# Optimization experiments

Hardware: AMD Instinct MI355X
Metric: run time of the kernel (lower is better)

## Reference

```python
import jax, jax.numpy as jnp
import numpy as np

B, S, D_IN, D_Q, D_V, H = 2, 2048, 1024, 1024, 1024, 16
HD_Q, HD_V = D_Q // H, D_V // H
SCALE = float(D_Q) ** 0.5  # source scales by sqrt(d_q), NOT sqrt(head_dim)


def setup_inputs() -> dict:
    key = jax.random.key(0)
    k1, k2, k3, k4, k5 = jax.random.split(key, 5)
    return {
        "x": jax.random.normal(k1, (B, S, D_IN), dtype=jnp.float32),
        "w_q": jax.random.normal(k2, (D_IN, D_Q), dtype=jnp.float32),
        "w_k": jax.random.normal(k3, (D_IN, D_Q), dtype=jnp.float32),
        "w_v": jax.random.normal(k4, (D_IN, D_V), dtype=jnp.float32),
        "W_o": jax.random.normal(k5, (D_IN, D_V), dtype=jnp.float32),
    }


def reference(x, w_q, w_k, w_v, W_o):
    b, s, _ = x.shape
    # projections: [b, s, d]
    q = x @ w_q
    k = x @ w_k
    v = x @ w_v
    # split heads -> [b, h, s, hd]
    Q = q.reshape(b, s, H, HD_Q).transpose(0, 2, 1, 3)
    K = k.reshape(b, s, H, HD_Q).transpose(0, 2, 1, 3)
    V = v.reshape(b, s, H, HD_V).transpose(0, 2, 1, 3)
    # full [b, h, s, s] score matrix (naive attention, as in source)
    scores = jnp.einsum("bhqd,bhkd->bhqk", Q, K)
    # FAITHFUL QUIRK: source applies softmax over dim=0 (batch axis)
    attn = jax.nn.softmax(scores / SCALE, axis=0)
    vals = jnp.einsum("bhqk,bhkd->bhqd", attn, V)
    vals = vals.transpose(0, 2, 1, 3).reshape(b, s, D_V)
    return vals @ W_o
```

## Files before the change

### kernel.cpp

```cpp
#include <hip/hip_runtime.h>


typedef _Float16 f16;
typedef __attribute__((ext_vector_type(8))) _Float16 f16x8;
typedef __attribute__((ext_vector_type(4))) _Float16 f16x4;
typedef __attribute__((ext_vector_type(4))) float f32x4;

#define MFMA16(a,b,c) __builtin_amdgcn_mfma_f32_16x16x32_f16(a,b,c,0,0,0)
#define GLD16(gp, lp) __builtin_amdgcn_global_load_lds(                         \
    (const __attribute__((address_space(1))) void*)(gp),                        \
    (__attribute__((address_space(3))) void*)(lp), 16, 0, 0)

__global__ __launch_bounds__(256) void prep(const float* __restrict__ x,
                                            const float* __restrict__ w0, const float* __restrict__ w1,
                                            const float* __restrict__ w2, const float* __restrict__ w3,
                                            f16* __restrict__ xh,
                                            f16* __restrict__ o0, f16* __restrict__ o1,
                                            f16* __restrict__ o2, f16* __restrict__ o3) {
    const int bb = blockIdx.x;
    const int tid = threadIdx.x;
    if (bb >= 1024) {
        int i = (bb - 1024) * 256 + tid;
        float4 v = ((const float4*)x)[i];
        f16x4 h;
        h[0] = (f16)v.x; h[1] = (f16)v.y; h[2] = (f16)v.z; h[3] = (f16)v.w;
        *(f16x4*)(xh + (long)i * 4) = h;
        return;
    }
    const float* w; f16* o;
    switch (bb & 3) {
        case 0: w = w0; o = o0; break;
        case 1: w = w1; o = o1; break;
        case 2: w = w2; o = o2; break;
        default: w = w3; o = o3; break;
    }
    __shared__ alignas(16) f16 t[64][72];
    const int d0 = ((bb >> 2) & 15) * 64, j0 = (bb >> 6) * 64;
    #pragma unroll
    for (int it = 0; it < 4; ++it) {
        int idx = it * 256 + tid;
        int row = idx >> 4, c4 = idx & 15;
        float4 v = *(const float4*)(w + (long)(d0 + row) * 1024 + j0 + c4 * 4);
        f16x4 h;
        h[0] = (f16)v.x; h[1] = (f16)v.y; h[2] = (f16)v.z; h[3] = (f16)v.w;
        *(f16x4*)&t[row][c4 * 4] = h;
    }
    __syncthreads();
    #pragma unroll
    for (int it = 0; it < 4; ++it) {
        int idx = it * 256 + tid;
        int jr = idx >> 4, d4 = idx & 15;
        f16x4 h;
        #pragma unroll
        for (int m = 0; m < 4; ++m) h[m] = t[d4 * 4 + m][jr];
        *(f16x4*)(o + (long)(j0 + jr) * 1024 + d0 + d4 * 4) = h;
    }
}

__global__ __launch_bounds__(256, 1) void gemm_qkv(const f16* __restrict__ A,
                                                   const f16* __restrict__ Wt,
                                                   f16* __restrict__ Qg,
                                                   f16* __restrict__ Kg,
                                                   f16* __restrict__ Vtg) {
    __shared__ alignas(16) f16 smem[16384];
    f16* As = smem;
    f16* Bs = smem + 8192;
    const int tid = threadIdx.x;
    const int wave = tid >> 6, lane = tid & 63;
    const int l15 = lane & 15, lq = lane >> 4;
    const int sw = l15 & 7;
    const int m0 = blockIdx.x * 128, n0 = blockIdx.y * 128;
    const int wr = (wave >> 1) * 64, wc = (wave & 1) * 64;
    const int r8 = lane >> 3;
    const int swc8 = ((lane & 7) ^ r8) * 8;

    f32x4 acc[4][4] = {};

    for (int kt = 0; kt < 16; ++kt) {
        __syncthreads();
        #pragma unroll
        for (int i = 0; i < 4; ++i) {
            GLD16(A  + (long)(m0 + wave * 32 + i * 8 + r8) * 1024 + kt * 64 + swc8, As + (wave * 32 + i * 8) * 64);
            GLD16(Wt + (long)(n0 + wave * 32 + i * 8 + r8) * 1024 + kt * 64 + swc8, Bs + (wave * 32 + i * 8) * 64);
        }
        __syncthreads();
        #pragma unroll
        for (int s2 = 0; s2 < 2; ++s2) {
            const int rc = ((s2 * 4 + lq) ^ sw) << 3;
            f16x8 af[4], bf[4];
            #pragma unroll
            for (int i = 0; i < 4; ++i) af[i] = *(const f16x8*)&As[(wr + i * 16 + l15) * 64 + rc];
            #pragma unroll
            for (int j = 0; j < 4; ++j) bf[j] = *(const f16x8*)&Bs[(wc + j * 16 + l15) * 64 + rc];
            #pragma unroll
            for (int i = 0; i < 4; ++i)
                #pragma unroll
                for (int j = 0; j < 4; ++j)
                    acc[i][j] = MFMA16(af[i], bf[j], acc[i][j]);
        }
    }

    const int sel = n0 >> 10;
    const int nb = n0 - (sel << 10);

    if (sel < 2) {
        f16* dst = sel == 0 ? Qg : Kg;
        const float qs = sel == 0 ? 0.045084219f : 1.0f;
        __syncthreads();
        #pragma unroll
        for (int i = 0; i < 4; ++i)
            #pragma unroll
            for (int j = 0; j < 4; ++j) {
                int row0 = wr + i * 16 + lq * 4;
                int colb = wc + j * 16 + l15;
                int chunk = colb >> 3, sub = colb & 7;
                #pragma unroll
                for (int r = 0; r < 4; ++r) {
                    int row = row0 + r;
                    smem[row * 128 + ((chunk ^ (row & 7)) << 3) + sub] = (f16)(acc[i][j][r] * qs);
                }
            }
        __syncthreads();
        #pragma unroll
        for (int e = 0; e < 8; ++e) {
            int id = e * 256 + tid;
            int row = id >> 4, c = id & 15;
            f16x8 v = *(const f16x8*)&smem[row * 128 + ((c ^ (row & 7)) << 3)];
            int gr = m0 + row, b = gr >> 11, s = gr & 2047;
            int gc = nb + c * 8, hh = gc >> 6, hd = gc & 63;
            *(f16x8*)(dst + (long)((b * 16 + hh) * 2048 + s) * 64 + hd) = v;
        }
    } else {
        #pragma unroll
        for (int i = 0; i < 4; ++i)
            #pragma unroll
            for (int j = 0; j < 4; ++j) {
                int gr0 = m0 + wr + i * 16 + lq * 4;
                int gc  = nb + wc + j * 16 + l15;
                int b = gr0 >> 11, s = gr0 & 2047;
                int hh = gc >> 6, hd = gc & 63;
                f16x4 v;
                #pragma unroll
                for (int r = 0; r < 4; ++r) v[r] = (f16)acc[i][j][r];
                *(f16x4*)(Vtg + (long)((b * 16 + hh) * 64 + hd) * 2048 + s) = v;
            }
    }
}

__global__ __launch_bounds__(256, 1) void gemm_out(const f16* __restrict__ A0,
                                                   const f16* __restrict__ A1,
                                                   const f16* __restrict__ Bt,
                                                   float* __restrict__ outp) {
    __shared__ alignas(16) f16 As[64][72];
    __shared__ alignas(16) f16 Bs[128][64];
    const int tid = threadIdx.x;
    const int wave = tid >> 6, lane = tid & 63;
    const int l15 = lane & 15, lq = lane >> 4;
    const int sw = l15 & 7;
    const int m0 = blockIdx.x * 64, n0 = blockIdx.y * 128;
    const int wr = (wave >> 1) * 32, wc = (wave & 1) * 64;
    const int r8 = lane >> 3;
    const int swc8 = ((lane & 7) ^ r8) * 8;

    f32x4 acc[2][4] = {};

    for (int kt = 0; kt < 16; ++kt) {
        __syncthreads();
        #pragma unroll
        for (int it = 0; it < 2; ++it) {
            int idx = it * 256 + tid;
            int row = idx >> 3, c = idx & 7;
            f16x8 a = *(const f16x8*)(A0 + (long)(m0 + row) * 1024 + kt * 64 + c * 8)
                    + *(const f16x8*)(A1 + (long)(m0 + row) * 1024 + kt * 64 + c * 8);
            *(f16x8*)&As[row][c * 8] = a;
        }
        #pragma unroll
        for (int i = 0; i < 4; ++i)
            GLD16(Bt + (long)(n0 + wave * 32 + i * 8 + r8) * 1024 + kt * 64 + swc8, &Bs[wave * 32 + i * 8][0]);
        __syncthreads();
        #pragma unroll
        for (int s2 = 0; s2 < 2; ++s2) {
            const int rc = ((s2 * 4 + lq) ^ sw) << 3;
            f16x8 af[2], bf[4];
            #pragma unroll
            for (int i = 0; i < 2; ++i) af[i] = *(const f16x8*)&As[wr + i * 16 + l15][s2 * 32 + lq * 8];
            #pragma unroll
            for (int j = 0; j < 4; ++j) bf[j] = *(const f16x8*)&Bs[wc + j * 16 + l15][rc];
            #pragma unroll
            for (int i = 0; i < 2; ++i)
                #pragma unroll
                for (int j = 0; j < 4; ++j)
                    acc[i][j] = MFMA16(af[i], bf[j], acc[i][j]);
        }
    }

    #pragma unroll
    for (int i = 0; i < 2; ++i)
        #pragma unroll
        for (int j = 0; j < 4; ++j) {
            int gr0 = m0 + wr + i * 16 + lq * 4;
            int gc  = n0 + wc + j * 16 + l15;
            #pragma unroll
            for (int r = 0; r < 4; ++r)
                outp[(long)(gr0 + r) * 1024 + gc] = acc[i][j][r];
        }
}

__global__ __launch_bounds__(256, 2) void attention_kernel(const f16* __restrict__ Qg,
                                                           const f16* __restrict__ Kg,
                                                           const f16* __restrict__ Vtg,
                                                           f16* __restrict__ vals0,
                                                           f16* __restrict__ vals1) {
    __shared__ alignas(16) f16 Ks [2][2][64][64];
    __shared__ alignas(16) f16 Vts[2][2][64][64];
    __shared__ alignas(16) f16 Ps [4][32][64];
    const int tid = threadIdx.x;
    const int wave = tid >> 6, lane = tid & 63;
    const int l15 = lane & 15, lq = lane >> 4;
    const int sw = l15 & 7;

    const int bid = blockIdx.x;
    const int xcd = bid & 7, sl = bid >> 3;
    const int h  = xcd * 2 + (sl & 1);
    const int qt = (sl >> 1) & 15, ks = sl >> 5;
    const int q0 = qt * 128, kt0 = ks * 16;
    f16* vals = ks ? vals1 : vals0;
    const int qr = q0 + wave * 32;

    f16x8 qfr[2][2][2];
    #pragma unroll
    for (int b2 = 0; b2 < 2; ++b2)
        #pragma unroll
        for (int qq = 0; qq < 2; ++qq)
            #pragma unroll
            for (int s2 = 0; s2 < 2; ++s2)
                qfr[b2][qq][s2] = *(const f16x8*)(Qg + (long)((b2 * 16 + h) * 2048 + qr + qq * 16 + l15) * 64
                                                  + s2 * 32 + lq * 8);

    f32x4 acc[2][2][4] = {};

    const int tb = wave & 1;
    const int r8 = lane >> 3;
    const int swc8 = ((lane & 7) ^ r8) * 8;
    const f16* kbase = Kg  + (long)((tb * 16 + h) * 2048 + kt0 * 64) * 64 + r8 * 64 + swc8;
    const f16* vbase = Vtg + (long)((tb * 16 + h) * 64 + r8) * 2048 + kt0 * 64 + swc8;

    auto stage = [&](int kt, int buf) {
        if (wave < 2) {
            const f16* g = kbase + kt * 4096;
            f16* l = &Ks[buf][tb][0][0];
            #pragma unroll
            for (int i = 0; i < 8; ++i) GLD16(g + i * 512, l + i * 512);
        } else {
            const f16* g = vbase + kt * 64;
            f16* l = &Vts[buf][tb][0][0];
            #pragma unroll
            for (int i = 0; i < 8; ++i) GLD16(g + (long)i * 8 * 2048, l + i * 512);
        }
    };

    stage(0, 0);
    for (int kt = 0; kt < 16; ++kt) {
        const int cur = kt & 1;
        __syncthreads();
        if (kt < 15) stage(kt + 1, cur ^ 1);

        f16x4 pp0[2][4], pp1[2][4];
        #pragma unroll
        for (int kf = 0; kf < 4; ++kf) {
            f32x4 S0[2] = {}, S1[2] = {};
            #pragma unroll
            for (int s2 = 0; s2 < 2; ++s2) {
                const int rc = ((s2 * 4 + lq) ^ sw) << 3;
                f16x8 a0 = *(const f16x8*)&Ks[cur][0][kf * 16 + l15][rc];
                f16x8 a1 = *(const f16x8*)&Ks[cur][1][kf * 16 + l15][rc];
                #pragma unroll
                for (int qq = 0; qq < 2; ++qq) {
                    S0[qq] = MFMA16(a0, qfr[0][qq][s2], S0[qq]);
                    S1[qq] = MFMA16(a1, qfr[1][qq][s2], S1[qq]);
                }
            }
            #pragma unroll
            for (int qq = 0; qq < 2; ++qq)
                #pragma unroll
                for (int r = 0; r < 4; ++r) {
                    float e = __builtin_amdgcn_exp2f(S1[qq][r] - S0[qq][r]);
                    float p = __builtin_amdgcn_rcpf(1.0f + e);
                    pp0[qq][kf][r] = (f16)p;
                    pp1[qq][kf][r] = (f16)(1.0f - p);
                }
        }

        const int pwsub = (lq & 1) << 2;
        #pragma unroll
        for (int pb = 0; pb < 2; ++pb) {
            #pragma unroll
            for (int qq = 0; qq < 2; ++qq)
                #pragma unroll
                for (int kf = 0; kf < 4; ++kf)
                    *(f16x4*)&Ps[wave][qq * 16 + l15][(((2 * kf + (lq >> 1)) ^ sw) << 3) + pwsub]
                        = pb ? pp1[qq][kf] : pp0[qq][kf];
            #pragma unroll
            for (int s2 = 0; s2 < 2; ++s2) {
                const int rc = ((s2 * 4 + lq) ^ sw) << 3;
                f16x8 pf[2], vf[4];
                #pragma unroll
                for (int qq = 0; qq < 2; ++qq)
                    pf[qq] = *(const f16x8*)&Ps[wave][qq * 16 + l15][rc];
                #pragma unroll
                for (int hf = 0; hf < 4; ++hf)
                    vf[hf] = *(const f16x8*)&Vts[cur][pb][hf * 16 + l15][rc];
                #pragma unroll
                for (int qq = 0; qq < 2; ++qq)
                    #pragma unroll
                    for (int hf = 0; hf < 4; ++hf)
                        acc[pb][qq][hf] = MFMA16(pf[qq], vf[hf], acc[pb][qq][hf]);
            }
        }
    }

    #pragma unroll
    for (int b2 = 0; b2 < 2; ++b2)
        #pragma unroll
        for (int qq = 0; qq < 2; ++qq)
            #pragma unroll
            for (int hf = 0; hf < 4; ++hf)
                #pragma unroll
                for (int r = 0; r < 4; ++r)
                    vals[(long)(b2 * 2048 + qr + qq * 16 + lq * 4 + r) * 1024 + h * 64 + hf * 16 + l15]
                        = (f16)acc[b2][qq][hf][r];
}

extern "C" void kernel_launch(void* const* d_in, const int* in_sizes, int n_in,
                              void* d_out, int out_size, void* d_ws, size_t ws_size,
                              hipStream_t stream) {
    const float* x  = (const float*)d_in[0];
    const float* wq = (const float*)d_in[1];
    const float* wk = (const float*)d_in[2];
    const float* wv = (const float*)d_in[3];
    const float* wo = (const float*)d_in[4];

    char* ws = (char*)d_ws;
    f16* xh    = (f16*)(ws);
    f16* wqT   = (f16*)(ws + 8388608);
    f16* wkT   = (f16*)(ws + 10485760);
    f16* wvT   = (f16*)(ws + 12582912);
    f16* woT   = (f16*)(ws + 14680064);
    f16* Qg    = (f16*)(ws + 16777216);
    f16* Kg    = (f16*)(ws + 25165824);
    f16* Vtg   = (f16*)(ws + 33554432);
    f16* vals1 = (f16*)(ws + 41943040);
    f16* vals0 = xh;
    (void)ws_size; (void)in_sizes; (void)n_in; (void)out_size;

    prep<<<5120, 256, 0, stream>>>(x, wq, wk, wv, wo, xh, wqT, wkT, wvT, woT);

    gemm_qkv<<<dim3(32, 24), 256, 0, stream>>>(xh, wqT, Qg, Kg, Vtg);

    attention_kernel<<<512, 256, 0, stream>>>(Qg, Kg, Vtg, vals0, vals1);

    gemm_out<<<dim3(64, 8), 256, 0, stream>>>(vals0, vals1, woT, (float*)d_out);
}
```

Before: 188.1 us.

## Split attention keys four ways with smaller key tiles and higher occupancy

Attention now splits the key dimension into four chunks instead of two when the workspace is large enough, launching twice as many blocks. The key tile shrinks from 64 to 32 keys, which halves the LDS footprint so launch bounds can target four blocks per CU. The P swizzle and staging loads are adapted to the narrower tiles. The output GEMM then sums four partial f16 value buffers instead of two, which adds extra global reads and f16 rounding of the partials. The four-way path depends on ws_size at runtime.

```diff
diff --git a/kernel.cpp b/kernel.cpp
--- a/kernel.cpp
+++ b/kernel.cpp
@@ -147,8 +147,11 @@
     }
 }
 
+template<int NSUM>
 __global__ __launch_bounds__(256, 1) void gemm_out(const f16* __restrict__ A0,
                                                    const f16* __restrict__ A1,
+                                                   const f16* __restrict__ A2,
+                                                   const f16* __restrict__ A3,
                                                    const f16* __restrict__ Bt,
                                                    float* __restrict__ outp) {
     __shared__ alignas(16) f16 As[64][72];
@@ -170,8 +173,10 @@
         for (int it = 0; it < 2; ++it) {
             int idx = it * 256 + tid;
             int row = idx >> 3, c = idx & 7;
-            f16x8 a = *(const f16x8*)(A0 + (long)(m0 + row) * 1024 + kt * 64 + c * 8)
-                    + *(const f16x8*)(A1 + (long)(m0 + row) * 1024 + kt * 64 + c * 8);
+            long off = (long)(m0 + row) * 1024 + kt * 64 + c * 8;
+            f16x8 a = *(const f16x8*)(A0 + off) + *(const f16x8*)(A1 + off);
+            if constexpr (NSUM == 4)
+                a = a + *(const f16x8*)(A2 + off) + *(const f16x8*)(A3 + off);
             *(f16x8*)&As[row][c * 8] = a;
         }
         #pragma unroll
@@ -206,25 +211,31 @@
         }
 }
 
-__global__ __launch_bounds__(256, 2) void attention_kernel(const f16* __restrict__ Qg,
+__global__ __launch_bounds__(256, 4) void attention_kernel(const f16* __restrict__ Qg,
                                                            const f16* __restrict__ Kg,
                                                            const f16* __restrict__ Vtg,
-                                                           f16* __restrict__ vals0,
-                                                           f16* __restrict__ vals1) {
-    __shared__ alignas(16) f16 Ks [2][2][64][64];
-    __shared__ alignas(16) f16 Vts[2][2][64][64];
-    __shared__ alignas(16) f16 Ps [4][32][64];
+                                                           f16* __restrict__ v0,
+                                                           f16* __restrict__ v1,
+                                                           f16* __restrict__ v2,
+                                                           f16* __restrict__ v3) {
+    __shared__ alignas(16) f16 Ks [2][2][32][64];
+    __shared__ alignas(16) f16 Vts[2][2][64][32];
+    __shared__ alignas(16) f16 Ps [4][32][32];
     const int tid = threadIdx.x;
     const int wave = tid >> 6, lane = tid & 63;
     const int l15 = lane & 15, lq = lane >> 4;
-    const int sw = l15 & 7;
-
+    const int sw  = l15 & 7;
+    const int psw = (l15 >> 1) & 3;
+
+    const int NS = gridDim.x >> 8;
+    const int nt = 64 / NS;
     const int bid = blockIdx.x;
     const int xcd = bid & 7, sl = bid >> 3;
     const int h  = xcd * 2 + (sl & 1);
     const int qt = (sl >> 1) & 15, ks = sl >> 5;
-    const int q0 = qt * 128, kt0 = ks * 16;
-    f16* vals = ks ? vals1 : vals0;
+    const int q0 = qt * 128;
+    const int key0 = ks * (nt << 5);
+    f16* vals = ks == 0 ? v0 : ks == 1 ? v1 : ks == 2 ? v2 : v3;
     const int qr = q0 + wave * 32;
 
     f16x8 qfr[2][2][2];
@@ -242,32 +253,32 @@
     const int tb = wave & 1;
     const int r8 = lane >> 3;
     const int swc8 = ((lane & 7) ^ r8) * 8;
-    const f16* kbase = Kg  + (long)((tb * 16 + h) * 2048 + kt0 * 64) * 64 + r8 * 64 + swc8;
-    const f16* vbase = Vtg + (long)((tb * 16 + h) * 64 + r8) * 2048 + kt0 * 64 + swc8;
+    const f16* kbase = Kg  + (long)((tb * 16 + h) * 2048 + key0) * 64 + r8 * 64 + swc8;
+    const f16* vbase = Vtg + (long)((tb * 16 + h) * 64 + (lane >> 2)) * 2048 + key0 + (lane & 3) * 8;
 
     auto stage = [&](int kt, int buf) {
         if (wave < 2) {
-            const f16* g = kbase + kt * 4096;
+            const f16* g = kbase + kt * 2048;
             f16* l = &Ks[buf][tb][0][0];
             #pragma unroll
-            for (int i = 0; i < 8; ++i) GLD16(g + i * 512, l + i * 512);
+            for (int i = 0; i < 4; ++i) GLD16(g + i * 512, l + i * 512);
         } else {
-            const f16* g = vbase + kt * 64;
+            const f16* g = vbase + kt * 32;
             f16* l = &Vts[buf][tb][0][0];
             #pragma unroll
-            for (int i = 0; i < 8; ++i) GLD16(g + (long)i * 8 * 2048, l + i * 512);
+            for (int i = 0; i < 4; ++i) GLD16(g + (long)i * 16 * 2048, l + i * 512);
         }
     };
 
     stage(0, 0);
-    for (int kt = 0; kt < 16; ++kt) {
+    for (int kt = 0; kt < nt; ++kt) {
         const int cur = kt & 1;
         __syncthreads();
-        if (kt < 15) stage(kt + 1, cur ^ 1);
-
-        f16x4 pp0[2][4], pp1[2][4];
-        #pragma unroll
-        for (int kf = 0; kf < 4; ++kf) {
+        if (kt < nt - 1) stage(kt + 1, cur ^ 1);
+
+        f16x4 pp0[2][2], pp1[2][2];
+        #pragma unroll
+        for (int kf = 0; kf < 2; ++kf) {
             f32x4 S0[2] = {}, S1[2] = {};
             #pragma unroll
             for (int s2 = 0; s2 < 2; ++s2) {
@@ -291,31 +302,27 @@
                 }
         }
 
-        const int pwsub = (lq & 1) << 2;
         #pragma unroll
         for (int pb = 0; pb < 2; ++pb) {
             #pragma unroll
             for (int qq = 0; qq < 2; ++qq)
                 #pragma unroll
-                for (int kf = 0; kf < 4; ++kf)
-                    *(f16x4*)&Ps[wave][qq * 16 + l15][(((2 * kf + (lq >> 1)) ^ sw) << 3) + pwsub]
+                for (int kf = 0; kf < 2; ++kf)
+                    *(f16x4*)&Ps[wave][qq * 16 + l15][((((kf << 1) | (lq >> 1)) ^ psw) << 3) + ((lq & 1) << 2)]
                         = pb ? pp1[qq][kf] : pp0[qq][kf];
-            #pragma unroll
-            for (int s2 = 0; s2 < 2; ++s2) {
-                const int rc = ((s2 * 4 + lq) ^ sw) << 3;
-                f16x8 pf[2], vf[4];
-                #pragma unroll
-                for (int qq = 0; qq < 2; ++qq)
-                    pf[qq] = *(const f16x8*)&Ps[wave][qq * 16 + l15][rc];
+            const int prc = (lq ^ psw) << 3;
+            f16x8 pf[2], vf[4];
+            #pragma unroll
+            for (int qq = 0; qq < 2; ++qq)
+                pf[qq] = *(const f16x8*)&Ps[wave][qq * 16 + l15][prc];
+            #pragma unroll
+            for (int hf = 0; hf < 4; ++hf)
+                vf[hf] = *(const f16x8*)&Vts[cur][pb][hf * 16 + l15][lq << 3];
+            #pragma unroll
+            for (int qq = 0; qq < 2; ++qq)
                 #pragma unroll
                 for (int hf = 0; hf < 4; ++hf)
-                    vf[hf] = *(const f16x8*)&Vts[cur][pb][hf * 16 + l15][rc];
-                #pragma unroll
-                for (int qq = 0; qq < 2; ++qq)
-                    #pragma unroll
-                    for (int hf = 0; hf < 4; ++hf)
-                        acc[pb][qq][hf] = MFMA16(pf[qq], vf[hf], acc[pb][qq][hf]);
-            }
+                    acc[pb][qq][hf] = MFMA16(pf[qq], vf[hf], acc[pb][qq][hf]);
         }
     }
 
@@ -350,14 +357,21 @@
     f16* Kg    = (f16*)(ws + 25165824);
     f16* Vtg   = (f16*)(ws + 33554432);
     f16* vals1 = (f16*)(ws + 41943040);
+    f16* vals2 = (f16*)(ws + 50331648);
+    f16* vals3 = (f16*)(ws + 58720256);
     f16* vals0 = xh;
-    (void)ws_size; (void)in_sizes; (void)n_in; (void)out_size;
+    (void)in_sizes; (void)n_in; (void)out_size;
+
+    const int NS = (ws_size >= (size_t)67108864) ? 4 : 2;
 
     prep<<<5120, 256, 0, stream>>>(x, wq, wk, wv, wo, xh, wqT, wkT, wvT, woT);
 
     gemm_qkv<<<dim3(32, 24), 256, 0, stream>>>(xh, wqT, Qg, Kg, Vtg);
 
-    attention_kernel<<<512, 256, 0, stream>>>(Qg, Kg, Vtg, vals0, vals1);
-
-    gemm_out<<<dim3(64, 8), 256, 0, stream>>>(vals0, vals1, woT, (float*)d_out);
-}
+    attention_kernel<<<NS * 256, 256, 0, stream>>>(Qg, Kg, Vtg, vals0, vals1, vals2, vals3);
+
+    if (NS == 4)
+        gemm_out<4><<<dim3(64, 8), 256, 0, stream>>>(vals0, vals1, vals2, vals3, woT, (float*)d_out);
+    else
+        gemm_out<2><<<dim3(64, 8), 256, 0, stream>>>(vals0, vals1, vals0, vals0, woT, (float*)d_out);
+}
```

Measured after the change: 281.4 us. 1.5x slower.
